# Performance work log

Measured on AMD Instinct MI355X. Metric: run time of the kernel, lower is better.

The kernel has to match this reference:

```python
import jax, jax.numpy as jnp
import numpy as np

N_NODES = 100000
N_EDGES = 1600000
N_GRAPHS = 512


def gcn_conv(x, src, dst, W, b, num_nodes):
    """PyG GCNConv: add self-loops, sym-normalize, aggregate, add bias."""
    xw = x @ W  # [N, out]
    # degree over destination nodes, +1 for the implicit self-loop
    deg = jax.ops.segment_sum(jnp.ones(src.shape[0], xw.dtype), dst,
                              num_segments=num_nodes) + 1.0
    dinv = jax.lax.rsqrt(deg)  # deg >= 1, safe
    norm = dinv[src] * dinv[dst]  # [E]
    agg = jax.ops.segment_sum(xw[src] * norm[:, None], dst,
                              num_segments=num_nodes)
    # self-loop contribution: dinv[i]^2 * xw[i]
    agg = agg + xw * (dinv * dinv)[:, None]
    return agg + b


def global_mean_pool(x, batch, num_graphs):
    sums = jax.ops.segment_sum(x, batch, num_segments=num_graphs)
    cnts = jax.ops.segment_sum(jnp.ones(x.shape[0], x.dtype), batch,
                               num_segments=num_graphs)
    return sums / jnp.maximum(cnts, 1.0)[:, None]


def setup_inputs() -> dict:
    key = jax.random.key(0)
    ks = jax.random.split(key, 9)
    x = jax.random.normal(ks[0], (N_NODES, 3), dtype=jnp.float32)
    edge_index = jax.random.randint(ks[1], (2, N_EDGES), 0, N_NODES, dtype=jnp.int64)
    batch = jnp.sort(jax.random.randint(ks[2], (N_NODES,), 0, N_GRAPHS, dtype=jnp.int64))
    W1 = jax.random.normal(ks[3], (3, 32), dtype=jnp.float32) * 0.5
    b1 = jax.random.normal(ks[4], (32,), dtype=jnp.float32) * 0.1
    W2 = jax.random.normal(ks[5], (32, 32), dtype=jnp.float32) * 0.2
    b2 = jax.random.normal(ks[6], (32,), dtype=jnp.float32) * 0.1
    Wl = jax.random.normal(ks[7], (32, 2), dtype=jnp.float32) * 0.2
    bl = jax.random.normal(ks[8], (2,), dtype=jnp.float32) * 0.1
    return {"x": x, "edge_index": edge_index, "batch": batch,
            "W1": W1, "b1": b1, "W2": W2, "b2": b2, "Wl": Wl, "bl": bl}


def reference(x, edge_index, batch, W1, b1, W2, b2, Wl, bl):
    src, dst = edge_index[0], edge_index[1]
    h = jax.nn.relu(gcn_conv(x, src, dst, W1, b1, N_NODES))
    h = jax.nn.relu(gcn_conv(h, src, dst, W2, b2, N_NODES))
    g = global_mean_pool(h, batch, N_GRAPHS)  # [G, 32]
    return g @ Wl + bl  # [G, 2]
```

## Files before the change

kernel.cpp:

```cpp
#include <hip/hip_runtime.h>
#include <hip/hip_fp16.h>

#define NN 100000
#define NE 1600000
#define NG 512
#define F  32

#define BSH    8
#define BNODES 256
#define NB     ((NN + BNODES - 1) / BNODES)
#define CAP    5120
#define PCHUNK 4096
#define NWGP   ((NE + PCHUNK - 1) / PCHUNK)

__global__ void k_partition(const int* __restrict__ src, const int* __restrict__ dst,
                            int* __restrict__ cursor, int* __restrict__ part) {
    __shared__ int hist[NB];
    __shared__ int base[NB];
    int tid = threadIdx.x;
    for (int i = tid; i < NB; i += 512) hist[i] = 0;
    __syncthreads();
    int e0 = blockIdx.x * PCHUNK;
    int e1 = min(e0 + PCHUNK, NE);
    for (int e = e0 + tid; e < e1; e += 512) atomicAdd(&hist[dst[e] >> BSH], 1);
    __syncthreads();
    for (int i = tid; i < NB; i += 512) {
        base[i] = hist[i] ? (i * CAP + atomicAdd(&cursor[i], hist[i])) : 0;
        hist[i] = 0;
    }
    __syncthreads();
    for (int e = e0 + tid; e < e1; e += 512) {
        int d = dst[e];
        int b = d >> BSH;
        int p = base[b] + atomicAdd(&hist[b], 1);
        part[p] = (src[e] << 8) | (d & (BNODES - 1));
    }
}

__global__ void k_fill2a(const int* __restrict__ part, const int* __restrict__ cursor,
                         const float* __restrict__ x,
                         int* __restrict__ rowpack, float* __restrict__ dinv,
                         float4* __restrict__ xd) {
    __shared__ int cnt[BNODES];
    __shared__ int lds[BNODES];
    int b = blockIdx.x, tid = threadIdx.x;
    int node0 = b << BSH;
    int s0 = b * CAP, s1 = s0 + cursor[b];
    cnt[tid] = 0;
    __syncthreads();
    for (int i = s0 + tid; i < s1; i += 256) atomicAdd(&cnt[part[i] & (BNODES - 1)], 1);
    __syncthreads();
    int c = cnt[tid];
    lds[tid] = c;
    __syncthreads();
    for (int o = 1; o < 256; o <<= 1) {
        int t = (tid >= o) ? lds[tid - o] : 0;
        __syncthreads();
        lds[tid] += t;
        __syncthreads();
    }
    int excl = lds[tid] - c;
    int n = node0 + tid;
    if (n < NN) {
        rowpack[n] = ((s0 + excl) << 10) | c;
        float d = rsqrtf((float)c + 1.0f);
        dinv[n] = d;
        xd[n] = make_float4(d * x[n * 3 + 0], d * x[n * 3 + 1], d * x[n * 3 + 2], d);
    }
}

__global__ void k_fill2b(const int* __restrict__ part, const int* __restrict__ cursor,
                         const int* __restrict__ rowpack, const float4* __restrict__ xd,
                         const float* __restrict__ W1, const float* __restrict__ b1,
                         int* __restrict__ csr, __half2* __restrict__ g1) {
    __shared__ int lcsr[CAP];
    __shared__ int off[BNODES];
    __shared__ float W1s[3 * F];
    __shared__ float b1s[F];
    int b = blockIdx.x, tid = threadIdx.x;
    int node0 = b << BSH;
    int s0 = b * CAP;
    int cnt = cursor[b];
    if (tid < 3 * F) W1s[tid] = W1[tid];
    if (tid < F) b1s[tid] = b1[tid];
    int n = node0 + tid;
    int pack = (n < NN) ? rowpack[n] : (s0 << 10);
    off[tid] = (pack >> 10) - s0;
    __syncthreads();
    for (int i = tid; i < cnt; i += 256) {
        int p = part[s0 + i];
        int pos = atomicAdd(&off[p & (BNODES - 1)], 1);
        lcsr[pos] = p >> 8;
    }
    __syncthreads();
    for (int i = tid; i < cnt; i += 256) csr[s0 + i] = lcsr[i];
    if (n < NN) {
        int deg = pack & 1023;
        int beg = (pack >> 10) - s0;
        int end = beg + deg;
        float ax = 0.0f, ay = 0.0f, az = 0.0f;
        int e = beg;
        for (; e + 3 < end; e += 4) {
            int i0 = lcsr[e], i1 = lcsr[e + 1], i2 = lcsr[e + 2], i3 = lcsr[e + 3];
            float4 v0 = xd[i0], v1 = xd[i1], v2 = xd[i2], v3 = xd[i3];
            ax += (v0.x + v1.x) + (v2.x + v3.x);
            ay += (v0.y + v1.y) + (v2.y + v3.y);
            az += (v0.z + v1.z) + (v2.z + v3.z);
        }
        for (; e < end; ++e) {
            float4 v = xd[lcsr[e]];
            ax += v.x; ay += v.y; az += v.z;
        }
        float4 sf = xd[n];
        float dn = sf.w;
        float cx = dn * (ax + sf.x), cy = dn * (ay + sf.y), cz = dn * (az + sf.z);
        __half2 tmp[16];
#pragma unroll
        for (int j = 0; j < 16; ++j) {
            int f0 = 2 * j, f1 = 2 * j + 1;
            float v0 = cx * W1s[f0] + cy * W1s[F + f0] + cz * W1s[2 * F + f0] + b1s[f0];
            float v1 = cx * W1s[f1] + cy * W1s[F + f1] + cz * W1s[2 * F + f1] + b1s[f1];
            tmp[j] = __floats2half2_rn(dn * fmaxf(v0, 0.0f), dn * fmaxf(v1, 0.0f));
        }
        uint4* hv = (uint4*)(g1 + (size_t)n * 16);
        const uint4* tv = (const uint4*)tmp;
        hv[0] = tv[0]; hv[1] = tv[1]; hv[2] = tv[2]; hv[3] = tv[3];
    }
}

__global__ void k_gather2p(const int* __restrict__ rowpack, const int* __restrict__ csr,
                           const __half2* __restrict__ g1, const float* __restrict__ dinv,
                           const int* __restrict__ batch,
                           const float* __restrict__ W2, const float* __restrict__ b2,
                           float* __restrict__ gsum) {
    __shared__ float W2s[F * F];
    __shared__ float b2s[F];
    __shared__ float ts[16][F];
    __shared__ float hs[16][F];
    __shared__ int bat[16];
    int tid = threadIdx.x;
    int nb = blockIdx.x * 16;
    for (int i = tid; i < F * F; i += 256) W2s[i] = W2[i];
    if (tid < F) b2s[tid] = b2[tid];
    if (tid < 16) bat[tid] = batch[nb + tid];
    int nl = tid >> 4, j = tid & 15;
    int n = nb + nl;
    {
        int pack = rowpack[n];
        int beg = pack >> 10, end = beg + (pack & 1023);
        float ax = 0.0f, ay = 0.0f;
        int e = beg;
        for (; e + 3 < end; e += 4) {
            int s0 = csr[e], s1 = csr[e + 1], s2 = csr[e + 2], s3 = csr[e + 3];
            float2 v0 = __half22float2(g1[s0 * 16 + j]);
            float2 v1 = __half22float2(g1[s1 * 16 + j]);
            float2 v2 = __half22float2(g1[s2 * 16 + j]);
            float2 v3 = __half22float2(g1[s3 * 16 + j]);
            ax += (v0.x + v1.x) + (v2.x + v3.x);
            ay += (v0.y + v1.y) + (v2.y + v3.y);
        }
        for (; e < end; ++e) {
            float2 v = __half22float2(g1[csr[e] * 16 + j]);
            ax += v.x; ay += v.y;
        }
        float dn = dinv[n];
        float2 sf = __half22float2(g1[n * 16 + j]);
        ts[nl][2 * j]     = dn * (ax + sf.x);
        ts[nl][2 * j + 1] = dn * (ay + sf.y);
    }
    __syncthreads();
    {
        int f = tid & 31;
        int nn0 = tid >> 5;
#pragma unroll
        for (int pass = 0; pass < 2; ++pass) {
            int nn = nn0 + pass * 8;
            float acc = b2s[f];
#pragma unroll
            for (int k = 0; k < F; ++k) acc += ts[nn][k] * W2s[k * F + f];
            hs[nn][f] = fmaxf(acc, 0.0f);
        }
    }
    __syncthreads();
    if (tid < F) {
        int g0 = bat[0], gmax = bat[15];
        for (int g = g0; g <= gmax; ++g) {
            float s = 0.0f;
#pragma unroll
            for (int i = 0; i < 16; ++i) if (bat[i] == g) s += hs[i][tid];
            atomicAdd(&gsum[g * F + tid], s);
        }
    }
}

__global__ void k_head(const float* __restrict__ gsum, const int* __restrict__ batch,
                       const float* __restrict__ Wl, const float* __restrict__ bl,
                       float* __restrict__ out) {
    int g = blockIdx.x * blockDim.x + threadIdx.x;
    if (g >= NG) return;
    int lo = 0, hi = NN;
    while (lo < hi) { int m = (lo + hi) >> 1; if (batch[m] < g) lo = m + 1; else hi = m; }
    int s = lo;
    lo = 0; hi = NN;
    while (lo < hi) { int m = (lo + hi) >> 1; if (batch[m] < g + 1) lo = m + 1; else hi = m; }
    float inv = 1.0f / fmaxf((float)(lo - s), 1.0f);
    float a0 = 0.0f, a1 = 0.0f;
#pragma unroll
    for (int k = 0; k < F; ++k) {
        float m = gsum[g * F + k] * inv;
        a0 += m * Wl[k * 2 + 0];
        a1 += m * Wl[k * 2 + 1];
    }
    out[g * 2 + 0] = a0 + bl[0];
    out[g * 2 + 1] = a1 + bl[1];
}

extern "C" void kernel_launch(void* const* d_in, const int* in_sizes, int n_in,
                              void* d_out, int out_size, void* d_ws, size_t ws_size,
                              hipStream_t stream) {
    const float* x     = (const float*)d_in[0];
    const int*   eidx  = (const int*)d_in[1];
    const int*   batch = (const int*)d_in[2];
    const float* W1    = (const float*)d_in[3];
    const float* b1    = (const float*)d_in[4];
    const float* W2    = (const float*)d_in[5];
    const float* b2    = (const float*)d_in[6];
    const float* Wl    = (const float*)d_in[7];
    const float* bl    = (const float*)d_in[8];
    float*       out   = (float*)d_out;

    const int* src = eidx;
    const int* dst = eidx + NE;

    char* base = (char*)d_ws;
    size_t off = 0;
    auto alloc = [&](size_t bytes) {
        void* p = base + off;
        off = (off + bytes + 127) & ~(size_t)127;
        return p;
    };
    int*     cursor  = (int*)alloc(NB * sizeof(int));
    int*     rowpack = (int*)alloc(NN * sizeof(int));
    int*     part    = (int*)alloc((size_t)NB * CAP * sizeof(int));
    int*     csr     = (int*)alloc((size_t)NB * CAP * sizeof(int));
    float*   dinv    = (float*)alloc(NN * sizeof(float));
    float4*  xd      = (float4*)alloc(NN * sizeof(float4));
    __half2* g1      = (__half2*)alloc((size_t)NN * 16 * sizeof(__half2));
    float*   gsum    = (float*)alloc((size_t)NG * F * sizeof(float));

    const int B = 256;
    const int gG16 = NN / 16;

    hipMemsetAsync(cursor, 0, NB * sizeof(int), stream);
    hipMemsetAsync(gsum, 0, (size_t)NG * F * sizeof(float), stream);

    k_partition<<<NWGP, 512, 0, stream>>>(src, dst, cursor, part);
    k_fill2a   <<<NB,   B,   0, stream>>>(part, cursor, x, rowpack, dinv, xd);
    k_fill2b   <<<NB,   B,   0, stream>>>(part, cursor, rowpack, xd, W1, b1, csr, g1);

    k_gather2p<<<gG16, B, 0, stream>>>(rowpack, csr, g1, dinv, batch, W2, b2, gsum);

    k_head<<<(NG + B - 1) / B, B, 0, stream>>>(gsum, batch, Wl, bl, out);
}
```

Measured before the change: 177.3 us.

## Locally sort partition chunk in LDS for coalesced bucket writes; merge memsets

The partition kernel now loads each edge once into registers, builds a per-bucket histogram, and does a block-wide prefix scan. It then sorts the packed edges by bucket in shared memory and writes them out contiguously per bucket, instead of scattering each edge straight to global memory. The aim is to coalesce the global writes to part and avoid reading src/dst twice. The two memsets are also merged into one by placing gsum right after cursor. The cost is more LDS use per block and extra barriers from the scan.

New measurement: 170.9 us. 3.6% less time.

```diff
diff --git a/kernel.cpp b/kernel.cpp
--- a/kernel.cpp
+++ b/kernel.cpp
@@ -11,29 +11,62 @@
 #define NB     ((NN + BNODES - 1) / BNODES)
 #define CAP    5120
 #define PCHUNK 4096
+#define EPT    8
 #define NWGP   ((NE + PCHUNK - 1) / PCHUNK)
 
 __global__ void k_partition(const int* __restrict__ src, const int* __restrict__ dst,
                             int* __restrict__ cursor, int* __restrict__ part) {
-    __shared__ int hist[NB];
-    __shared__ int base[NB];
+    __shared__ int   s_cnt[NB];
+    __shared__ int   s_scan[512];
+    __shared__ int   s_lstart[NB];
+    __shared__ int   s_base[NB];
+    __shared__ int   lsort[PCHUNK];
+    __shared__ short lbkt[PCHUNK];
     int tid = threadIdx.x;
-    for (int i = tid; i < NB; i += 512) hist[i] = 0;
+    for (int i = tid; i < NB; i += 512) s_cnt[i] = 0;
     __syncthreads();
     int e0 = blockIdx.x * PCHUNK;
     int e1 = min(e0 + PCHUNK, NE);
-    for (int e = e0 + tid; e < e1; e += 512) atomicAdd(&hist[dst[e] >> BSH], 1);
-    __syncthreads();
-    for (int i = tid; i < NB; i += 512) {
-        base[i] = hist[i] ? (i * CAP + atomicAdd(&cursor[i], hist[i])) : 0;
-        hist[i] = 0;
-    }
-    __syncthreads();
-    for (int e = e0 + tid; e < e1; e += 512) {
-        int d = dst[e];
-        int b = d >> BSH;
-        int p = base[b] + atomicAdd(&hist[b], 1);
-        part[p] = (src[e] << 8) | (d & (BNODES - 1));
+    int pk[EPT]; short bk[EPT];
+    int m = 0;
+#pragma unroll
+    for (int k = 0; k < EPT; ++k) {
+        int e = e0 + tid + k * 512;
+        if (e < e1) {
+            int d = dst[e];
+            pk[m] = (src[e] << 8) | (d & (BNODES - 1));
+            bk[m] = (short)(d >> BSH);
+            atomicAdd(&s_cnt[bk[m]], 1);
+            ++m;
+        }
+    }
+    __syncthreads();
+    int cv = (tid < NB) ? s_cnt[tid] : 0;
+    s_scan[tid] = cv;
+    __syncthreads();
+    for (int o = 1; o < 512; o <<= 1) {
+        int t = (tid >= o) ? s_scan[tid - o] : 0;
+        __syncthreads();
+        s_scan[tid] += t;
+        __syncthreads();
+    }
+    if (tid < NB) {
+        s_lstart[tid] = s_scan[tid] - cv;
+        if (cv) s_base[tid] = tid * CAP + atomicAdd(&cursor[tid], cv);
+        s_cnt[tid] = 0;
+    }
+    __syncthreads();
+    for (int k = 0; k < m; ++k) {
+        int b = bk[k];
+        int r = s_lstart[b] + atomicAdd(&s_cnt[b], 1);
+        lsort[r] = pk[k];
+        lbkt[r]  = (short)b;
+    }
+    __syncthreads();
+    int cnt = e1 - e0;
+    for (int i = tid; i < cnt; i += 512) {
+        int b = lbkt[i];
+        part[s_base[b] + (i - s_lstart[b])] = lsort[i];
     }
 }
 
@@ -239,20 +272,19 @@
         off = (off + bytes + 127) & ~(size_t)127;
         return p;
     };
-    int*     cursor  = (int*)alloc(NB * sizeof(int));
+    int*     cursor  = (int*)alloc(NB * sizeof(int) + (size_t)NG * F * sizeof(float));
+    float*   gsum    = (float*)(cursor + NB);
     int*     rowpack = (int*)alloc(NN * sizeof(int));
     int*     part    = (int*)alloc((size_t)NB * CAP * sizeof(int));
     int*     csr     = (int*)alloc((size_t)NB * CAP * sizeof(int));
     float*   dinv    = (float*)alloc(NN * sizeof(float));
     float4*  xd      = (float4*)alloc(NN * sizeof(float4));
     __half2* g1      = (__half2*)alloc((size_t)NN * 16 * sizeof(__half2));
-    float*   gsum    = (float*)alloc((size_t)NG * F * sizeof(float));
 
     const int B = 256;
     const int gG16 = NN / 16;
 
-    hipMemsetAsync(cursor, 0, NB * sizeof(int), stream);
-    hipMemsetAsync(gsum, 0, (size_t)NG * F * sizeof(float), stream);
+    hipMemsetAsync(cursor, 0, NB * sizeof(int) + (size_t)NG * F * sizeof(float), stream);
 
     k_partition<<<NWGP, 512, 0, stream>>>(src, dst, cursor, part);
     k_fill2a   <<<NB,   B,   0, stream>>>(part, cursor, x, rowpack, dinv, xd);
```
